# Optimization experiments

Hardware: AMD Instinct MI355X
Metric: run time of the kernel (lower is better)

The kernel has to match this reference:

```python
import jax, jax.numpy as jnp
import numpy as np


def setup_inputs() -> dict:
    key = jax.random.key(0)
    ks = jax.random.split(key, 6)
    B, T, D, E, F = 2, 2048, 1024, 8, 2048
    x = jax.random.normal(ks[0], (B, T, D), dtype=jnp.float32)
    gate_w = jax.random.normal(ks[1], (D, E), dtype=jnp.float32) * (1.0 / np.sqrt(D))
    base_w1 = jax.random.normal(ks[2], (D, F), dtype=jnp.float32) * np.sqrt(2.0 / (D + F))
    base_w2 = jax.random.normal(ks[3], (F, D), dtype=jnp.float32) * np.sqrt(2.0 / (F + D))
    expert_w1 = base_w1[None] + jax.random.normal(ks[4], (E, D, F), dtype=jnp.float32) * 0.01
    expert_w2 = base_w2[None] + jax.random.normal(ks[5], (E, F, D), dtype=jnp.float32) * 0.01
    expert_b1 = jnp.zeros((E, F), dtype=jnp.float32)
    expert_b2 = jnp.zeros((E, D), dtype=jnp.float32)
    return {"x": x, "gate_w": gate_w, "expert_w1": expert_w1, "expert_b1": expert_b1,
            "expert_w2": expert_w2, "expert_b2": expert_b2}


def reference(x, gate_w, expert_w1, expert_b1, expert_w2, expert_b2):
    # Router (TopKRouter): top-2 routing with aux load-balance loss + z-loss
    E = gate_w.shape[-1]
    TOP_K = 2
    Z_LOSS_COEF = 1e-3
    logits = jnp.einsum('btd,de->bte', x, gate_w)                       # [B,T,E]
    top_vals, top_idx = jax.lax.top_k(logits, TOP_K)                    # [B,T,K]
    router_weights = jax.nn.softmax(top_vals, axis=-1)                  # [B,T,K]
    probs = jax.nn.softmax(logits, axis=-1)
    mask = jax.nn.one_hot(top_idx[..., 0], E, dtype=x.dtype)            # top-1 expert mask
    tokens_per_expert = mask.mean(axis=(0, 1))                          # [E]
    router_prob_per_expert = probs.mean(axis=(0, 1))                    # [E]
    aux_loss = E * jnp.sum(tokens_per_expert * router_prob_per_expert) \
               + jnp.mean(logits ** 2) * Z_LOSS_COEF

    # Expert FFNs: compute all experts densely, then gather top-k outputs.
    # (Same math as per-token weight gather, without the BTDF intermediate.)
    h = jnp.einsum('btd,edf->btef', x, expert_w1) + expert_b1           # [B,T,E,F]
    h = jax.nn.gelu(h, approximate=False)                               # torch F.gelu default = erf
    out_all = jnp.einsum('btef,efd->bted', h, expert_w2) + expert_b2    # [B,T,E,D]
    gathered = jnp.take_along_axis(out_all, top_idx[..., None], axis=2) # [B,T,K,D]
    output = jnp.einsum('btk,btkd->btd', router_weights, gathered)      # [B,T,D]
    return output, aux_loss
```

## Files before the change

kernel.cpp:

```cpp
#include <hip/hip_runtime.h>
#include <hip/hip_bf16.h>

#define NTOK 4096
#define DDIM 1024
#define NEXP 8
#define FDIM 2048
#define CAP  4096
#define RTOK 32
#define MT   16

typedef float f32x4 __attribute__((ext_vector_type(4)));
typedef short s16x8 __attribute__((ext_vector_type(8)));
typedef short s16x4 __attribute__((ext_vector_type(4)));

__device__ __forceinline__ unsigned short f2bf(float f) {
  unsigned int u = __float_as_uint(f);
  unsigned int r = u + 0x7fffu + ((u >> 16) & 1u);
  return (unsigned short)(r >> 16);
}

__device__ __forceinline__ void gload16(const void* g, void* l) {
  __builtin_amdgcn_global_load_lds(
      (__attribute__((address_space(1))) unsigned int*)(g),
      (__attribute__((address_space(3))) unsigned int*)(l), 16, 0, 0);
}

__device__ __forceinline__ void transpose_tile(const float* __restrict__ src,
                                               unsigned short* __restrict__ dst,
                                               int R, int C, int c0, int r0, int e,
                                               char* smem, int tid) {
  float (*tile)[68] = (float(*)[68])smem;
  const float* s = src + (size_t)e * R * C;
  unsigned short* d = dst + (size_t)e * R * C;
  const int lr = tid >> 4, lc = (tid & 15) * 4;
  #pragma unroll
  for (int p = 0; p < 4; p++) {
    float4 v = *(const float4*)(s + (size_t)(r0 + p * 16 + lr) * C + c0 + lc);
    tile[p * 16 + lr][lc]     = v.x;
    tile[p * 16 + lr][lc + 1] = v.y;
    tile[p * 16 + lr][lc + 2] = v.z;
    tile[p * 16 + lr][lc + 3] = v.w;
  }
  __syncthreads();
  const int sc = tid >> 3, sr = (tid & 7) * 8;
  #pragma unroll
  for (int p = 0; p < 2; p++) {
    int c = p * 32 + sc;
    s16x8 o;
    #pragma unroll
    for (int j = 0; j < 8; j++) o[j] = (short)f2bf(tile[sr + j][c]);
    *(s16x8*)(d + (size_t)(c0 + c) * R + r0 + sr) = o;
  }
}

__global__ __launch_bounds__(256)
void k_prep(const float* __restrict__ x, const float* __restrict__ gw,
            const float* __restrict__ w1, const float* __restrict__ w2,
            unsigned short* __restrict__ xb, unsigned short* __restrict__ w1t,
            unsigned short* __restrict__ w2t,
            float* __restrict__ topw, int* __restrict__ elist,
            int* __restrict__ ecnt, int* __restrict__ cnt1,
            float* __restrict__ psum, float* __restrict__ sqsum) {
  __shared__ char smem[68864];
  const int bid = blockIdx.x, tid = threadIdx.x;

  if (bid < 4096) {
    int cx = bid & 31, ry = (bid >> 5) & 15, e = bid >> 9;
    transpose_tile(w1, w1t, DDIM, FDIM, cx * 64, ry * 64, e, smem, tid);
    return;
  }
  if (bid < 8192) {
    int b = bid - 4096;
    int cx = b & 15, ry = (b >> 4) & 31, e = b >> 9;
    transpose_tile(w2, w2t, FDIM, DDIM, cx * 64, ry * 64, e, smem, tid);
    return;
  }

  float (*gwt)[DDIM + 4] = (float(*)[DDIM + 4])smem;
  float (*xs)[264]       = (float(*)[264])(smem + 32896);
  double (*lgd)[NEXP]    = (double(*)[NEXP])(smem + 66688);
  float* bps = (float*)(smem + 68736);
  int*   bc  = (int*)(smem + 68768);
  float* bsq = (float*)(smem + 68800);
  const int tok0 = (bid - 8192) * RTOK;

  for (int i = tid; i < DDIM * NEXP; i += 256) {
    int d = i >> 3, e = i & 7;
    gwt[e][d] = gw[i];
  }
  if (tid < NEXP) { bps[tid] = 0.f; bc[tid] = 0; }
  if (tid == 0) *bsq = 0.f;

  const int t = tid >> 3, e = tid & 7;
  double a0 = 0.0, a1 = 0.0, a2 = 0.0, a3 = 0.0;
  for (int c = 0; c < DDIM; c += 256) {
    __syncthreads();
    for (int i = tid; i < RTOK * 64; i += 256) {
      int r = i >> 6, c4 = i & 63;
      float4 v = *(const float4*)(x + (size_t)(tok0 + r) * DDIM + c + c4 * 4);
      *(float4*)&xs[r][c4 * 4] = v;
      s16x4 o;
      o[0] = (short)f2bf(v.x); o[1] = (short)f2bf(v.y);
      o[2] = (short)f2bf(v.z); o[3] = (short)f2bf(v.w);
      *(s16x4*)(xb + (size_t)(tok0 + r) * DDIM + c + c4 * 4) = o;
    }
    __syncthreads();
    #pragma unroll 8
    for (int d4 = 0; d4 < 64; d4++) {
      float4 xv = *(const float4*)&xs[t][d4 * 4];
      float4 gv = *(const float4*)&gwt[e][c + d4 * 4];
      a0 += (double)xv.x * (double)gv.x;
      a1 += (double)xv.y * (double)gv.y;
      a2 += (double)xv.z * (double)gv.z;
      a3 += (double)xv.w * (double)gv.w;
    }
  }
  lgd[t][e] = (a0 + a1) + (a2 + a3);
  __syncthreads();

  if (tid < RTOK) {
    int tok = tok0 + tid;
    double acc[NEXP];
    #pragma unroll
    for (int k = 0; k < NEXP; k++) acc[k] = lgd[tid][k];
    int i0 = 0; double v0 = acc[0];
    #pragma unroll
    for (int k = 1; k < NEXP; k++) if (acc[k] > v0) { v0 = acc[k]; i0 = k; }
    int i1 = (i0 == 0) ? 1 : 0; double v1 = acc[i1];
    #pragma unroll
    for (int k = 0; k < NEXP; k++) if (k != i0 && acc[k] > v1) { v1 = acc[k]; i1 = k; }
    float w0 = 1.0f / (1.0f + expf((float)(v1 - v0)));
    topw[2*tok] = w0; topw[2*tok + 1] = 1.0f - w0;
    int s0 = atomicAdd(&ecnt[i0], 1); elist[i0*CAP + s0] = 2*tok;
    int s1 = atomicAdd(&ecnt[i1], 1); elist[i1*CAP + s1] = 2*tok + 1;
    atomicAdd(&bc[i0], 1);
    float lm = (float)acc[0];
    #pragma unroll
    for (int k = 1; k < NEXP; k++) lm = fmaxf(lm, (float)acc[k]);
    float pe[NEXP], ps = 0.f, sq = 0.f;
    #pragma unroll
    for (int k = 0; k < NEXP; k++) {
      float le = (float)acc[k];
      pe[k] = expf(le - lm); ps += pe[k];
      sq += le * le;
    }
    float inv = 1.0f / ps;
    #pragma unroll
    for (int k = 0; k < NEXP; k++) atomicAdd(&bps[k], pe[k] * inv);
    atomicAdd(bsq, sq);
  }
  __syncthreads();
  if (tid < NEXP) { atomicAdd(&psum[tid], bps[tid]); atomicAdd(&cnt1[tid], bc[tid]); }
  if (tid == 0) atomicAdd(sqsum, *bsq);
}

template<int K, int N, bool GELU, bool ROWSHIFT>
__global__ __launch_bounds__(512)
void k_gemm(const unsigned short* __restrict__ A, const unsigned short* __restrict__ Bt,
            const float* __restrict__ bias, void* __restrict__ Out,
            const int* __restrict__ elist, const int* __restrict__ ecnt) {
  constexpr int BM = 128, BN = 128, BK = 128, WM = 2, WN = 4;
  constexpr int GX = N / BN;
  constexpr int TOT = GX * MT * NEXP;
  constexpr int CHUNK = TOT / 8;
  constexpr int AISS = BM / 32;
  constexpr int BISS = BN / 32;
  constexpr int MF = BM / WM / 16;
  constexpr int NF = BN / WN / 16;
  __shared__ unsigned char lsA[BM * 256];
  __shared__ unsigned char lsB[BN * 256];

  const int w = blockIdx.x;
  const int swz = (w & 7) * CHUNK + (w >> 3);
  const int e = swz / (GX * MT);
  const int loc = swz % (GX * MT);
  const int mt = loc % MT, nt = loc / MT;

  const int cnt = ecnt[e];
  const int m0 = mt * BM;
  if (m0 >= cnt) return;
  const int rv = min(BM, cnt - m0);
  const int* lst = elist + e * CAP + m0;
  const int tid = threadIdx.x, wv = tid >> 6, lane = tid & 63;
  const int wm = wv / WN, wn = wv % WN;
  const unsigned short* Be = Bt + (size_t)e * N * K;

  const unsigned short* agp[AISS];
  const unsigned short* bgp[BISS];
  int adst[AISS], bdst[BISS];
  const int cu = tid & 15;
  #pragma unroll
  for (int li = 0; li < AISS; li++) {
    int r = li * 32 + (tid >> 4);
    int rr = (r < rv) ? r : 0;
    int aid = lst[rr];
    int arow = ROWSHIFT ? (aid >> 1) : aid;
    int csrc = (cu ^ (r & 15)) * 16;
    agp[li] = A + (size_t)arow * K + (csrc >> 1);
    adst[li] = r * 256 + cu * 16;
  }
  #pragma unroll
  for (int li = 0; li < BISS; li++) {
    int r = li * 32 + (tid >> 4);
    int csrc = (cu ^ (r & 15)) * 16;
    bgp[li] = Be + (size_t)(nt * BN + r) * K + (csrc >> 1);
    bdst[li] = r * 256 + cu * 16;
  }

  f32x4 acc[MF][NF];
  #pragma unroll
  for (int mi = 0; mi < MF; mi++)
    #pragma unroll
    for (int ni = 0; ni < NF; ni++)
      acc[mi][ni] = (f32x4){0.f, 0.f, 0.f, 0.f};

  constexpr int NK = K / BK;
  for (int t = 0; t < NK; ++t) {
    const int k0 = t * BK;
    #pragma unroll
    for (int li = 0; li < AISS; li++) gload16(agp[li] + k0, &lsA[adst[li]]);
    #pragma unroll
    for (int li = 0; li < BISS; li++) gload16(bgp[li] + k0, &lsB[bdst[li]]);
    __syncthreads();
    #pragma unroll
    for (int ks = 0; ks < 4; ks++) {
      s16x8 af[MF], bf[NF];
      #pragma unroll
      for (int mi = 0; mi < MF; mi++) {
        int row = wm * (BM / WM) + mi * 16 + (lane & 15);
        int c16 = (ks * 4 + (lane >> 4)) ^ (row & 15);
        af[mi] = *(const s16x8*)&lsA[row * 256 + c16 * 16];
      }
      #pragma unroll
      for (int ni = 0; ni < NF; ni++) {
        int row = wn * (BN / WN) + ni * 16 + (lane & 15);
        int c16 = (ks * 4 + (lane >> 4)) ^ (row & 15);
        bf[ni] = *(const s16x8*)&lsB[row * 256 + c16 * 16];
      }
      #pragma unroll
      for (int mi = 0; mi < MF; mi++)
        #pragma unroll
        for (int ni = 0; ni < NF; ni++)
          acc[mi][ni] = __builtin_amdgcn_mfma_f32_16x16x32_bf16(af[mi], bf[ni], acc[mi][ni], 0, 0, 0);
    }
    __syncthreads();
  }

  const int g4 = (lane >> 4) * 4, cn = lane & 15;
  #pragma unroll
  for (int mi = 0; mi < MF; mi++) {
    #pragma unroll
    for (int reg = 0; reg < 4; reg++) {
      int r = wm * (BM / WM) + mi * 16 + g4 + reg;
      if (r < rv) {
        int aid = lst[r];
        #pragma unroll
        for (int ni = 0; ni < NF; ni++) {
          int n = nt * BN + wn * (BN / WN) + ni * 16 + cn;
          float v = acc[mi][ni][reg] + bias[(size_t)e * N + n];
          if constexpr (GELU) {
            v = 0.5f * v * (1.0f + erff(v * 0.70710678118654752f));
            ((unsigned short*)Out)[(size_t)aid * N + n] = f2bf(v);
          } else {
            ((float*)Out)[(size_t)aid * N + n] = v;
          }
        }
      }
    }
  }
}

__global__ void k_combine(const float* __restrict__ buf, const float* __restrict__ topw,
                          float* __restrict__ out,
                          const int* __restrict__ cnt1, const float* __restrict__ psum,
                          const float* __restrict__ sqsum) {
  int i = blockIdx.x * 256 + threadIdx.x;
  int t = i >> 8, c = i & 255;
  float w0 = topw[2*t], w1 = topw[2*t + 1];
  float4 a = ((const float4*)(buf + (size_t)(2*t) * DDIM))[c];
  float4 b = ((const float4*)(buf + (size_t)(2*t + 1) * DDIM))[c];
  float4 o;
  o.x = w0*a.x + w1*b.x; o.y = w0*a.y + w1*b.y;
  o.z = w0*a.z + w1*b.z; o.w = w0*a.w + w1*b.w;
  ((float4*)out)[i] = o;
  if (i == 0) {
    float s = 0.f;
    for (int e = 0; e < NEXP; e++)
      s += ((float)cnt1[e] / (float)NTOK) * (psum[e] / (float)NTOK);
    out[(size_t)NTOK * DDIM] = (float)NEXP * s + (*sqsum) / (float)(NTOK * NEXP) * 1e-3f;
  }
}

extern "C" void kernel_launch(void* const* d_in, const int* in_sizes, int n_in,
                              void* d_out, int out_size, void* d_ws, size_t ws_size,
                              hipStream_t stream) {
  const float* x  = (const float*)d_in[0];
  const float* gw = (const float*)d_in[1];
  const float* w1 = (const float*)d_in[2];
  const float* b1 = (const float*)d_in[3];
  const float* w2 = (const float*)d_in[4];
  const float* b2 = (const float*)d_in[5];
  float* out = (float*)d_out;
  char* p = (char*)d_ws;

  int*   ecnt  = (int*)p;
  int*   cnt1  = (int*)(p + 32);
  float* psum  = (float*)(p + 64);
  float* sqsum = (float*)(p + 96);
  float* topw  = (float*)(p + 256);
  int*   elist = (int*)(p + 256 + 32768);
  unsigned short* xb  = (unsigned short*)(p + 256 + 32768 + 131072);
  unsigned short* w1t = xb  + (size_t)NTOK * DDIM;
  unsigned short* w2t = w1t + (size_t)NEXP * DDIM * FDIM;
  unsigned short* Hb  = w2t + (size_t)NEXP * DDIM * FDIM;
  float* obuf = (float*)(Hb + (size_t)NTOK * 2 * FDIM);

  hipMemsetAsync(p, 0, 128, stream);
  k_prep<<<8192 + NTOK / RTOK, 256, 0, stream>>>(x, gw, w1, w2, xb, w1t, w2t,
                                                 topw, elist, ecnt, cnt1, psum, sqsum);
  k_gemm<DDIM, FDIM, true,  true ><<<(FDIM/128)*MT*NEXP, 512, 0, stream>>>(xb, w1t, b1, Hb, elist, ecnt);
  k_gemm<FDIM, DDIM, false, false><<<(DDIM/128)*MT*NEXP, 512, 0, stream>>>(Hb, w2t, b2, obuf, elist, ecnt);
  k_combine<<<NTOK * DDIM / 4 / 256, 256, 0, stream>>>(obuf, topw, out, cnt1, psum, sqsum);
}
```

Before: 249.2 us.

## Move w2 transpose into GEMM1 launch and coarsen w1 transpose blocks

The fp32-to-bf16 transpose of expert_w2 moves out of the prep kernel and into a new fused GEMM1 kernel. Extra blocks in that launch do the transpose while the other blocks run the first expert GEMM, so the w2 conversion can overlap with GEMM1 compute. The w1 transpose blocks now each handle four 64x64 tiles, using register prefetch and a double-buffered LDS tile, which cuts the block count from 4096 to 1024. In exchange, the GEMM1 code is duplicated into a specialised kernel, and half the threads sit idle in the 512-thread transpose blocks.

```diff
diff --git a/kernel.cpp b/kernel.cpp
--- a/kernel.cpp
+++ b/kernel.cpp
@@ -25,54 +25,55 @@
       (__attribute__((address_space(3))) unsigned int*)(l), 16, 0, 0);
 }
 
-__device__ __forceinline__ void transpose_tile(const float* __restrict__ src,
-                                               unsigned short* __restrict__ dst,
-                                               int R, int C, int c0, int r0, int e,
-                                               char* smem, int tid) {
-  float (*tile)[68] = (float(*)[68])smem;
-  const float* s = src + (size_t)e * R * C;
-  unsigned short* d = dst + (size_t)e * R * C;
-  const int lr = tid >> 4, lc = (tid & 15) * 4;
-  #pragma unroll
-  for (int p = 0; p < 4; p++) {
-    float4 v = *(const float4*)(s + (size_t)(r0 + p * 16 + lr) * C + c0 + lc);
-    tile[p * 16 + lr][lc]     = v.x;
-    tile[p * 16 + lr][lc + 1] = v.y;
-    tile[p * 16 + lr][lc + 2] = v.z;
-    tile[p * 16 + lr][lc + 3] = v.w;
-  }
-  __syncthreads();
-  const int sc = tid >> 3, sr = (tid & 7) * 8;
-  #pragma unroll
-  for (int p = 0; p < 2; p++) {
-    int c = p * 32 + sc;
-    s16x8 o;
-    #pragma unroll
-    for (int j = 0; j < 8; j++) o[j] = (short)f2bf(tile[sr + j][c]);
-    *(s16x8*)(d + (size_t)(c0 + c) * R + r0 + sr) = o;
-  }
-}
-
 __global__ __launch_bounds__(256)
 void k_prep(const float* __restrict__ x, const float* __restrict__ gw,
-            const float* __restrict__ w1, const float* __restrict__ w2,
+            const float* __restrict__ w1,
             unsigned short* __restrict__ xb, unsigned short* __restrict__ w1t,
-            unsigned short* __restrict__ w2t,
             float* __restrict__ topw, int* __restrict__ elist,
             int* __restrict__ ecnt, int* __restrict__ cnt1,
             float* __restrict__ psum, float* __restrict__ sqsum) {
   __shared__ char smem[68864];
   const int bid = blockIdx.x, tid = threadIdx.x;
 
-  if (bid < 4096) {
-    int cx = bid & 31, ry = (bid >> 5) & 15, e = bid >> 9;
-    transpose_tile(w1, w1t, DDIM, FDIM, cx * 64, ry * 64, e, smem, tid);
-    return;
-  }
-  if (bid < 8192) {
-    int b = bid - 4096;
-    int cx = b & 15, ry = (b >> 4) & 31, e = b >> 9;
-    transpose_tile(w2, w2t, FDIM, DDIM, cx * 64, ry * 64, e, smem, tid);
+  if (bid >= 128) {
+    const int b = bid - 128;
+    const int cx = b & 31, ry = (b >> 5) & 3, e = b >> 7;
+    const int c0 = cx * 64, r0b = ry * 256;
+    float (*tile)[64][65] = (float(*)[64][65])smem;
+    const float* s = w1 + (size_t)e * DDIM * FDIM;
+    unsigned short* d = w1t + (size_t)e * DDIM * FDIM;
+    const int lr = tid >> 4, lc = (tid & 15) * 4;
+    const int sc = tid >> 3, sr = (tid & 7) * 8;
+    float4 v[4];
+    #pragma unroll
+    for (int p = 0; p < 4; p++)
+      v[p] = *(const float4*)(s + (size_t)(r0b + p * 16 + lr) * FDIM + c0 + lc);
+    #pragma unroll
+    for (int t = 0; t < 4; t++) {
+      const int cur = t & 1;
+      #pragma unroll
+      for (int p = 0; p < 4; p++) {
+        tile[cur][p * 16 + lr][lc]     = v[p].x;
+        tile[cur][p * 16 + lr][lc + 1] = v[p].y;
+        tile[cur][p * 16 + lr][lc + 2] = v[p].z;
+        tile[cur][p * 16 + lr][lc + 3] = v[p].w;
+      }
+      if (t < 3) {
+        #pragma unroll
+        for (int p = 0; p < 4; p++)
+          v[p] = *(const float4*)(s + (size_t)(r0b + (t + 1) * 64 + p * 16 + lr) * FDIM + c0 + lc);
+      }
+      __syncthreads();
+      const int r0 = r0b + t * 64;
+      #pragma unroll
+      for (int p = 0; p < 2; p++) {
+        int c = p * 32 + sc;
+        s16x8 o;
+        #pragma unroll
+        for (int j = 0; j < 8; j++) o[j] = (short)f2bf(tile[cur][sr + j][c]);
+        *(s16x8*)(d + (size_t)(c0 + c) * DDIM + r0 + sr) = o;
+      }
+    }
     return;
   }
 
@@ -82,7 +83,7 @@
   float* bps = (float*)(smem + 68736);
   int*   bc  = (int*)(smem + 68768);
   float* bsq = (float*)(smem + 68800);
-  const int tok0 = (bid - 8192) * RTOK;
+  const int tok0 = bid * RTOK;
 
   for (int i = tid; i < DDIM * NEXP; i += 256) {
     int d = i >> 3, e = i & 7;
@@ -152,6 +153,163 @@
   __syncthreads();
   if (tid < NEXP) { atomicAdd(&psum[tid], bps[tid]); atomicAdd(&cnt1[tid], bc[tid]); }
   if (tid == 0) atomicAdd(sqsum, *bsq);
+}
+
+__global__ __launch_bounds__(512)
+void k_gemm1w2(const unsigned short* __restrict__ A, const unsigned short* __restrict__ Bt,
+               const float* __restrict__ bias, unsigned short* __restrict__ Out,
+               const int* __restrict__ elist, const int* __restrict__ ecnt,
+               const float* __restrict__ w2, unsigned short* __restrict__ w2t) {
+  __shared__ char smem[65536];
+  const int bid = blockIdx.x, tid = threadIdx.x;
+
+  if (bid < 1024) {
+    float (*tile)[64][65] = (float(*)[64][65])smem;
+    const int cx = bid & 15, ry = (bid >> 4) & 7, e = bid >> 7;
+    const int c0 = cx * 64, r0b = ry * 256;
+    const float* s = w2 + (size_t)e * FDIM * DDIM;
+    unsigned short* d = w2t + (size_t)e * FDIM * DDIM;
+    const bool act = tid < 256;
+    const int lr = (tid >> 4) & 15, lc = (tid & 15) * 4;
+    const int sc = (tid >> 3) & 31, sr = (tid & 7) * 8;
+    float4 v[4];
+    if (act) {
+      #pragma unroll
+      for (int p = 0; p < 4; p++)
+        v[p] = *(const float4*)(s + (size_t)(r0b + p * 16 + lr) * DDIM + c0 + lc);
+    }
+    #pragma unroll
+    for (int t = 0; t < 4; t++) {
+      const int cur = t & 1;
+      if (act) {
+        #pragma unroll
+        for (int p = 0; p < 4; p++) {
+          tile[cur][p * 16 + lr][lc]     = v[p].x;
+          tile[cur][p * 16 + lr][lc + 1] = v[p].y;
+          tile[cur][p * 16 + lr][lc + 2] = v[p].z;
+          tile[cur][p * 16 + lr][lc + 3] = v[p].w;
+        }
+        if (t < 3) {
+          #pragma unroll
+          for (int p = 0; p < 4; p++)
+            v[p] = *(const float4*)(s + (size_t)(r0b + (t + 1) * 64 + p * 16 + lr) * DDIM + c0 + lc);
+        }
+      }
+      __syncthreads();
+      if (act) {
+        const int r0 = r0b + t * 64;
+        #pragma unroll
+        for (int p = 0; p < 2; p++) {
+          int c = p * 32 + sc;
+          s16x8 o;
+          #pragma unroll
+          for (int j = 0; j < 8; j++) o[j] = (short)f2bf(tile[cur][sr + j][c]);
+          *(s16x8*)(d + (size_t)(c0 + c) * FDIM + r0 + sr) = o;
+        }
+      }
+    }
+    return;
+  }
+
+  constexpr int K = DDIM, N = FDIM;
+  constexpr int BM = 128, BN = 128, BK = 128, WM = 2, WN = 4;
+  constexpr int GX = N / BN, CHUNK = GX * MT;
+  constexpr int AISS = 4, BISS = 4, MF = 4, NF = 2;
+  unsigned char* lsA = (unsigned char*)smem;
+  unsigned char* lsB = (unsigned char*)smem + 32768;
+
+  const int w = bid - 1024;
+  const int swz = (w & 7) * CHUNK + (w >> 3);
+  const int e = swz / CHUNK;
+  const int loc = swz % CHUNK;
+  const int mt = loc % MT, nt = loc / MT;
+
+  const int cnt = ecnt[e];
+  const int m0 = mt * BM;
+  if (m0 >= cnt) return;
+  const int rv = min(BM, cnt - m0);
+  const int* lst = elist + e * CAP + m0;
+  const int wv = tid >> 6, lane = tid & 63;
+  const int wm = wv / WN, wn = wv % WN;
+  const unsigned short* Be = Bt + (size_t)e * N * K;
+
+  const unsigned short* agp[AISS];
+  const unsigned short* bgp[BISS];
+  int adst[AISS], bdst[BISS];
+  const int cu = tid & 15;
+  #pragma unroll
+  for (int li = 0; li < AISS; li++) {
+    int r = li * 32 + (tid >> 4);
+    int rr = (r < rv) ? r : 0;
+    int aid = lst[rr];
+    int arow = aid >> 1;
+    agp[li] = A + (size_t)arow * K + (cu ^ (r & 15)) * 8;
+    adst[li] = r * 256 + cu * 16;
+  }
+  #pragma unroll
+  for (int li = 0; li < BISS; li++) {
+    int r = li * 32 + (tid >> 4);
+    bgp[li] = Be + (size_t)(nt * BN + r) * K + (cu ^ (r & 15)) * 8;
+    bdst[li] = r * 256 + cu * 16;
+  }
+
+  f32x4 acc[MF][NF];
+  #pragma unroll
+  for (int mi = 0; mi < MF; mi++)
+    #pragma unroll
+    for (int ni = 0; ni < NF; ni++)
+      acc[mi][ni] = (f32x4){0.f, 0.f, 0.f, 0.f};
+
+  constexpr int NK = K / BK;
+  for (int t = 0; t < NK; ++t) {
+    const int k0 = t * BK;
+    #pragma unroll
+    for (int li = 0; li < AISS; li++) gload16(agp[li] + k0, &lsA[adst[li]]);
+    #pragma unroll
+    for (int li = 0; li < BISS; li++) gload16(bgp[li] + k0, &lsB[bdst[li]]);
+    __syncthreads();
+    #pragma unroll
+    for (int ks = 0; ks < 4; ks++) {
+      s16x8 af[MF], bf[NF];
+      #pragma unroll
+      for (int mi = 0; mi < MF; mi++) {
+        int row = wm * (BM / WM) + mi * 16 + (lane & 15);
+        int c16 = (ks * 4 + (lane >> 4)) ^ (row & 15);
+        af[mi] = *(const s16x8*)&lsA[row * 256 + c16 * 16];
+      }
+      #pragma unroll
+      for (int ni = 0; ni < NF; ni++) {
+        int row = wn * (BN / WN) + ni * 16 + (lane & 15);
+        int c16 = (ks * 4 + (lane >> 4)) ^ (row & 15);
+        bf[ni] = *(const s16x8*)&lsB[row * 256 + c16 * 16];
+      }
+      #pragma unroll
+      for (int mi = 0; mi < MF; mi++)
+        #pragma unroll
+        for (int ni = 0; ni < NF; ni++)
+          acc[mi][ni] = __builtin_amdgcn_mfma_f32_16x16x32_bf16(af[mi], bf[ni], acc[mi][ni], 0, 0, 0);
+    }
+    __syncthreads();
+  }
+
+  const int g4 = (lane >> 4) * 4, cn = lane & 15;
+  #pragma unroll
+  for (int mi = 0; mi < MF; mi++) {
+    #pragma unroll
+    for (int reg = 0; reg < 4; reg++) {
+      int r = wm * (BM / WM) + mi * 16 + g4 + reg;
+      if (r < rv) {
+        int aid = lst[r];
+        #pragma unroll
+        for (int ni = 0; ni < NF; ni++) {
+          int n = nt * BN + wn * (BN / WN) + ni * 16 + cn;
+          float v = acc[mi][ni][reg] + bias[(size_t)e * N + n];
+          v = 0.5f * v * (1.0f + erff(v * 0.70710678118654752f));
+          Out[(size_t)aid * N + n] = f2bf(v);
+        }
+      }
+    }
+  }
 }
 
 template<int K, int N, bool GELU, bool ROWSHIFT>
@@ -163,10 +321,8 @@
   constexpr int GX = N / BN;
   constexpr int TOT = GX * MT * NEXP;
   constexpr int CHUNK = TOT / 8;
-  constexpr int AISS = BM / 32;
-  constexpr int BISS = BN / 32;
-  constexpr int MF = BM / WM / 16;
-  constexpr int NF = BN / WN / 16;
+  constexpr int AISS = BM / 32, BISS = BN / 32;
+  constexpr int MF = BM / WM / 16, NF = BN / WN / 16;
   __shared__ unsigned char lsA[BM * 256];
   __shared__ unsigned char lsB[BN * 256];
 
@@ -195,15 +351,13 @@
     int rr = (r < rv) ? r : 0;
     int aid = lst[rr];
     int arow = ROWSHIFT ? (aid >> 1) : aid;
-    int csrc = (cu ^ (r & 15)) * 16;
-    agp[li] = A + (size_t)arow * K + (csrc >> 1);
+    agp[li] = A + (size_t)arow * K + (cu ^ (r & 15)) * 8;
     adst[li] = r * 256 + cu * 16;
   }
   #pragma unroll
   for (int li = 0; li < BISS; li++) {
     int r = li * 32 + (tid >> 4);
-    int csrc = (cu ^ (r & 15)) * 16;
-    bgp[li] = Be + (size_t)(nt * BN + r) * K + (csrc >> 1);
+    bgp[li] = Be + (size_t)(nt * BN + r) * K + (cu ^ (r & 15)) * 8;
     bdst[li] = r * 256 + cu * 16;
   }
 
@@ -316,9 +470,9 @@
   float* obuf = (float*)(Hb + (size_t)NTOK * 2 * FDIM);
 
   hipMemsetAsync(p, 0, 128, stream);
-  k_prep<<<8192 + NTOK / RTOK, 256, 0, stream>>>(x, gw, w1, w2, xb, w1t, w2t,
-                                                 topw, elist, ecnt, cnt1, psum, sqsum);
-  k_gemm<DDIM, FDIM, true,  true ><<<(FDIM/128)*MT*NEXP, 512, 0, stream>>>(xb, w1t, b1, Hb, elist, ecnt);
+  k_prep<<<128 + 1024, 256, 0, stream>>>(x, gw, w1, xb, w1t,
+                                         topw, elist, ecnt, cnt1, psum, sqsum);
+  k_gemm1w2<<<1024 + 2048, 512, 0, stream>>>(xb, w1t, b1, Hb, elist, ecnt, w2, w2t);
   k_gemm<FDIM, DDIM, false, false><<<(DDIM/128)*MT*NEXP, 512, 0, stream>>>(Hb, w2t, b2, obuf, elist, ecnt);
   k_combine<<<NTOK * DDIM / 4 / 256, 256, 0, stream>>>(obuf, topw, out, cnt1, psum, sqsum);
 }
```

Result: faster. 239.6 us (-3.8%).
